# Kernel optimization log

Hardware: AMD Instinct MI355X
Metric: run time of the kernel (lower is better)

Reference implementation:

```python
import jax, jax.numpy as jnp
import numpy as np

H = 128            # hidden_size; also the chunk length from torch.split(x, hidden_size)
NUM_CHUNKS = 4096  # B
INPUT_SIZE = 1
NUM_CLASSES = 1


def setup_inputs() -> dict:
    key = jax.random.key(0)
    ks = jax.random.split(key, 7)
    N = NUM_CHUNKS * H
    s = 1.0 / np.sqrt(H).astype(np.float32)
    x = jax.random.normal(ks[0], (N,), dtype=jnp.float32)
    W_ih = jax.random.uniform(ks[1], (4 * H, INPUT_SIZE), minval=-s, maxval=s, dtype=jnp.float32)
    W_hh = jax.random.uniform(ks[2], (4 * H, H), minval=-s, maxval=s, dtype=jnp.float32)
    b_ih = jax.random.uniform(ks[3], (4 * H,), minval=-s, maxval=s, dtype=jnp.float32)
    b_hh = jax.random.uniform(ks[4], (4 * H,), minval=-s, maxval=s, dtype=jnp.float32)
    fc_W = jax.random.uniform(ks[5], (NUM_CLASSES, H), minval=-s, maxval=s, dtype=jnp.float32)
    fc_b = jax.random.uniform(ks[6], (NUM_CLASSES,), minval=-s, maxval=s, dtype=jnp.float32)
    return {"x": x, "W_ih": W_ih, "W_hh": W_hh, "b_ih": b_ih, "b_hh": b_hh,
            "fc_W": fc_W, "fc_b": fc_b}


def reference(x, W_ih, W_hh, b_ih, b_hh, fc_W, fc_b):
    # Original: split flat x into chunks of length H, run each chunk as a
    # batch-1 LSTM (input_size=1), take final hidden state, apply fc_out.
    # Here all chunks are batched into one fused recurrent pass.
    Hh = W_hh.shape[1]
    xb = x.reshape(-1, Hh, 1)                                  # [B, T=H, 1]
    # input projection is time-parallel: precompute gate pre-activations
    pre = jnp.einsum('bti,gi->btg', xb, W_ih) + b_ih + b_hh    # [B, T, 4H]

    def step(carry, p_t):
        h, c = carry                                           # [B, H] each
        gates = p_t + h @ W_hh.T                               # [B, 4H]
        i, f, g, o = jnp.split(gates, 4, axis=-1)              # PyTorch gate order i,f,g,o
        i = jax.nn.sigmoid(i)
        f = jax.nn.sigmoid(f)
        g = jnp.tanh(g)
        o = jax.nn.sigmoid(o)
        c = f * c + i * g
        h = o * jnp.tanh(c)
        return (h, c), None

    B = xb.shape[0]
    h0 = jnp.zeros((B, Hh), dtype=x.dtype)
    c0 = jnp.zeros((B, Hh), dtype=x.dtype)
    (hT, _), _ = jax.lax.scan(step, (h0, c0), jnp.swapaxes(pre, 0, 1))
    return hT @ fc_W.T + fc_b                                  # [B, num_classes]
```

## Files before the change

kernel.cpp:

```cpp
#include <hip/hip_runtime.h>


#define H   128
#define T   128
#define MB  16
#define BLOCK 512
#define HSTRIDE 136
#define XSTRIDE 20

typedef _Float16 f16x8 __attribute__((ext_vector_type(8)));
typedef float    f32x4 __attribute__((ext_vector_type(4)));

__global__ void prep_whh_kernel(const float* __restrict__ W_hh, _Float16* __restrict__ wfrag)
{
    int idx = blockIdx.x * blockDim.x + threadIdx.x;
    int l15 =  idx        & 15;
    int q   = (idx >> 4)  & 3;
    int kc  = (idx >> 6)  & 3;
    int g   = (idx >> 8)  & 3;
    int ct  = (idx >> 10) & 7;
    int n  = g * H + ct * 16 + l15;
    int k0 = kc * 32 + q * 8;
    const float* src = W_hh + (size_t)n * H + k0;
    f16x8 f;
    #pragma unroll
    for (int i = 0; i < 8; ++i) f[i] = (_Float16)src[i];
    *(f16x8*)(wfrag + (size_t)idx * 8) = f;
}

__device__ __forceinline__ float frcp(float v) { return __builtin_amdgcn_rcpf(v); }

__launch_bounds__(BLOCK, 2)
__global__ void lstm_fused_kernel(const float* __restrict__ x,
                                  const float* __restrict__ W_ih,
                                  const _Float16* __restrict__ wfrag,
                                  const float* __restrict__ b_ih,
                                  const float* __restrict__ b_hh,
                                  const float* __restrict__ fc_W,
                                  const float* __restrict__ fc_b,
                                  float* __restrict__ out)
{
    __shared__ __align__(16) float xs[T + 1][XSTRIDE];
    __shared__ __align__(16) _Float16 hbuf[2][MB][HSTRIDE];

    const int tid  = threadIdx.x;
    const int wave = tid >> 6;
    const int lane = tid & 63;
    const int l15  = lane & 15;
    const int q    = lane >> 4;
    const int jcol = wave * 16 + l15;

    {
        const int t0 = tid & 127;
        const int b0 = (tid >> 7) * 4;
        const float* xb = x + (size_t)blockIdx.x * (MB * T);
        #pragma unroll
        for (int bb = 0; bb < 4; ++bb)
            xs[t0][b0 + bb] = xb[(b0 + bb) * T + t0];
    }
    for (int i = tid; i < MB * HSTRIDE; i += BLOCK)
        (&hbuf[0][0][0])[i] = (_Float16)0.0f;

    f16x8 wf[4][4];
    {
        const _Float16* wbase = wfrag + (size_t)wave * (4 * 4 * 4 * 16 * 8);
        #pragma unroll
        for (int g = 0; g < 4; ++g)
            #pragma unroll
            for (int kc = 0; kc < 4; ++kc)
                wf[g][kc] = *(const f16x8*)(wbase + ((((g * 4 + kc) * 4 + q) * 16 + l15) * 8));
    }

    float wih[4], bias[4];
    #pragma unroll
    for (int g = 0; g < 4; ++g) {
        const int n = g * H + jcol;
        wih[g]  = W_ih[n];
        bias[g] = b_ih[n] + b_hh[n];
    }

    float c0[4] = {0.f, 0.f, 0.f, 0.f};

    __syncthreads();

    f32x4 initv[4];
    {
        float4 xl = *(const float4*)&xs[0][q * 4];
        #pragma unroll
        for (int g = 0; g < 4; ++g) {
            initv[g][0] = fmaf(xl.x, wih[g], bias[g]);
            initv[g][1] = fmaf(xl.y, wih[g], bias[g]);
            initv[g][2] = fmaf(xl.z, wih[g], bias[g]);
            initv[g][3] = fmaf(xl.w, wih[g], bias[g]);
        }
    }

    for (int t = 0; t < T; ++t) {
        #pragma unroll
        for (int g = 0; g < 4; ++g)
            #pragma unroll
            for (int kc = 0; kc < 4; ++kc)
                asm volatile("" : "+v"(wf[g][kc]));

        const int rb = t & 1;
        const int wb = rb ^ 1;

        f16x8 af[4];
        #pragma unroll
        for (int kc = 0; kc < 4; ++kc)
            af[kc] = *(const f16x8*)&hbuf[rb][l15][kc * 32 + q * 8];

        f32x4 acc[4];
        #pragma unroll
        for (int g = 0; g < 4; ++g)
            acc[g] = __builtin_amdgcn_mfma_f32_16x16x32_f16(af[0], wf[g][0], initv[g], 0, 0, 0);
        #pragma unroll
        for (int kc = 1; kc < 4; ++kc)
            #pragma unroll
            for (int g = 0; g < 4; ++g)
                acc[g] = __builtin_amdgcn_mfma_f32_16x16x32_f16(af[kc], wf[g][kc], acc[g], 0, 0, 0);

        {
            float4 xl = *(const float4*)&xs[t + 1][q * 4];
            #pragma unroll
            for (int g = 0; g < 4; ++g) {
                initv[g][0] = fmaf(xl.x, wih[g], bias[g]);
                initv[g][1] = fmaf(xl.y, wih[g], bias[g]);
                initv[g][2] = fmaf(xl.z, wih[g], bias[g]);
                initv[g][3] = fmaf(xl.w, wih[g], bias[g]);
            }
        }

        #pragma unroll
        for (int r = 0; r < 4; ++r) {
            const int b = q * 4 + r;
            float ai = acc[0][r], afv = acc[1][r], ag = acc[2][r], ao = acc[3][r];
            float Ei = __expf(-ai);
            float Ef = __expf(-afv);
            float Eg = __expf(2.0f * ag);
            float u  = 1.0f + Ei;
            float v  = 1.0f + Ef;
            float w  = 1.0f + Eg;
            float wm = Eg - 1.0f;
            float uw = u * w;
            float cn = fmaf(c0[r], uw, wm * v) * frcp(v * uw);
            c0[r] = cn;
            float Eo = __expf(-ao);
            float Ec = __expf(2.0f * cn);
            float hv = (Ec - 1.0f) * frcp((Ec + 1.0f) * (1.0f + Eo));
            hbuf[wb][b][jcol] = (_Float16)hv;
        }
        __syncthreads();
    }

    if (tid < 256) {
        const int b    = tid >> 4;
        const int part = tid & 15;
        const _Float16* hrow = &hbuf[0][b][0];
        float s = 0.0f;
        #pragma unroll
        for (int i = 0; i < 8; ++i) {
            const int j = part * 8 + i;
            s += fc_W[j] * (float)hrow[j];
        }
        s += __shfl_xor(s, 8, 16);
        s += __shfl_xor(s, 4, 16);
        s += __shfl_xor(s, 2, 16);
        s += __shfl_xor(s, 1, 16);
        if (part == 0)
            out[blockIdx.x * MB + b] = s + fc_b[0];
    }
}

extern "C" void kernel_launch(void* const* d_in, const int* in_sizes, int n_in,
                              void* d_out, int out_size, void* d_ws, size_t ws_size,
                              hipStream_t stream)
{
    const float* x    = (const float*)d_in[0];
    const float* W_ih = (const float*)d_in[1];
    const float* W_hh = (const float*)d_in[2];
    const float* b_ih = (const float*)d_in[3];
    const float* b_hh = (const float*)d_in[4];
    const float* fc_W = (const float*)d_in[5];
    const float* fc_b = (const float*)d_in[6];
    float* out = (float*)d_out;

    _Float16* wfrag = (_Float16*)d_ws;

    hipLaunchKernelGGL(prep_whh_kernel, dim3(32), dim3(256), 0, stream, W_hh, wfrag);

    const int B = in_sizes[0] / H;
    dim3 grid(B / MB);
    dim3 block(BLOCK);
    hipLaunchKernelGGL(lstm_fused_kernel, grid, block, 0, stream,
                       x, W_ih, wfrag, b_ih, b_hh, fc_W, fc_b, out);
}
```

Baseline: 173.8 us.

## Halve batch rows per block and dedupe per-lane gate math

Each block now handles 8 batch rows instead of 16, which doubles the grid so more blocks are resident per CU to hide the serial recurrence latency. The 16-row MFMA tile reads duplicated h rows, so half of the matrix math is wasted. The gate nonlinearities are deduplicated so each lane updates 2 cells instead of 4, shortening the per-step elementwise chain. Launch bounds are raised to 4 blocks per CU and the register-pinning asm on the weight fragments is removed, which risks spilling the 64 registers of resident weight fragments under the tighter register budget.

```diff
diff --git a/kernel.cpp b/kernel.cpp
--- a/kernel.cpp
+++ b/kernel.cpp
@@ -3,10 +3,10 @@
 
 #define H   128
 #define T   128
-#define MB  16
+#define MB  8
 #define BLOCK 512
 #define HSTRIDE 136
-#define XSTRIDE 20
+#define XSTRIDE 12
 
 typedef _Float16 f16x8 __attribute__((ext_vector_type(8)));
 typedef float    f32x4 __attribute__((ext_vector_type(4)));
@@ -30,7 +30,7 @@
 
 __device__ __forceinline__ float frcp(float v) { return __builtin_amdgcn_rcpf(v); }
 
-__launch_bounds__(BLOCK, 2)
+__launch_bounds__(BLOCK, 4)
 __global__ void lstm_fused_kernel(const float* __restrict__ x,
                                   const float* __restrict__ W_ih,
                                   const _Float16* __restrict__ wfrag,
@@ -50,13 +50,15 @@
     const int q    = lane >> 4;
     const int jcol = wave * 16 + l15;
 
+    const int r0 = (q >> 1) * 2;
+    const int b0 = (q * 4 + r0) & 7;
+
     {
         const int t0 = tid & 127;
-        const int b0 = (tid >> 7) * 4;
+        const int bb = tid >> 7;
         const float* xb = x + (size_t)blockIdx.x * (MB * T);
-        #pragma unroll
-        for (int bb = 0; bb < 4; ++bb)
-            xs[t0][b0 + bb] = xb[(b0 + bb) * T + t0];
+        xs[t0][bb]     = xb[bb * T + t0];
+        xs[t0][bb + 4] = xb[(bb + 4) * T + t0];
     }
     for (int i = tid; i < MB * HSTRIDE; i += BLOCK)
         (&hbuf[0][0][0])[i] = (_Float16)0.0f;
@@ -79,36 +81,27 @@
         bias[g] = b_ih[n] + b_hh[n];
     }
 
-    float c0[4] = {0.f, 0.f, 0.f, 0.f};
+    float c0 = 0.f, c1 = 0.f;
 
     __syncthreads();
 
     f32x4 initv[4];
     {
-        float4 xl = *(const float4*)&xs[0][q * 4];
-        #pragma unroll
-        for (int g = 0; g < 4; ++g) {
-            initv[g][0] = fmaf(xl.x, wih[g], bias[g]);
-            initv[g][1] = fmaf(xl.y, wih[g], bias[g]);
-            initv[g][2] = fmaf(xl.z, wih[g], bias[g]);
-            initv[g][3] = fmaf(xl.w, wih[g], bias[g]);
-        }
+        #pragma unroll
+        for (int g = 0; g < 4; ++g)
+            #pragma unroll
+            for (int r = 0; r < 4; ++r)
+                initv[g][r] = fmaf(xs[0][(q * 4 + r) & 7], wih[g], bias[g]);
     }
 
     for (int t = 0; t < T; ++t) {
-        #pragma unroll
-        for (int g = 0; g < 4; ++g)
-            #pragma unroll
-            for (int kc = 0; kc < 4; ++kc)
-                asm volatile("" : "+v"(wf[g][kc]));
-
         const int rb = t & 1;
         const int wb = rb ^ 1;
 
         f16x8 af[4];
         #pragma unroll
         for (int kc = 0; kc < 4; ++kc)
-            af[kc] = *(const f16x8*)&hbuf[rb][l15][kc * 32 + q * 8];
+            af[kc] = *(const f16x8*)&hbuf[rb][l15 & 7][kc * 32 + q * 8];
 
         f32x4 acc[4];
         #pragma unroll
@@ -120,20 +113,14 @@
             for (int g = 0; g < 4; ++g)
                 acc[g] = __builtin_amdgcn_mfma_f32_16x16x32_f16(af[kc], wf[g][kc], acc[g], 0, 0, 0);
 
+        #pragma unroll
+        for (int g = 0; g < 4; ++g)
+            #pragma unroll
+            for (int r = 0; r < 4; ++r)
+                initv[g][r] = fmaf(xs[t + 1][(q * 4 + r) & 7], wih[g], bias[g]);
+
         {
-            float4 xl = *(const float4*)&xs[t + 1][q * 4];
-            #pragma unroll
-            for (int g = 0; g < 4; ++g) {
-                initv[g][0] = fmaf(xl.x, wih[g], bias[g]);
-                initv[g][1] = fmaf(xl.y, wih[g], bias[g]);
-                initv[g][2] = fmaf(xl.z, wih[g], bias[g]);
-                initv[g][3] = fmaf(xl.w, wih[g], bias[g]);
-            }
-        }
-
-        #pragma unroll
-        for (int r = 0; r < 4; ++r) {
-            const int b = q * 4 + r;
+            const int r = r0;
             float ai = acc[0][r], afv = acc[1][r], ag = acc[2][r], ao = acc[3][r];
             float Ei = __expf(-ai);
             float Ef = __expf(-afv);
@@ -143,17 +130,35 @@
             float w  = 1.0f + Eg;
             float wm = Eg - 1.0f;
             float uw = u * w;
-            float cn = fmaf(c0[r], uw, wm * v) * frcp(v * uw);
-            c0[r] = cn;
+            float cn = fmaf(c0, uw, wm * v) * frcp(v * uw);
+            c0 = cn;
             float Eo = __expf(-ao);
             float Ec = __expf(2.0f * cn);
             float hv = (Ec - 1.0f) * frcp((Ec + 1.0f) * (1.0f + Eo));
-            hbuf[wb][b][jcol] = (_Float16)hv;
+            hbuf[wb][b0][jcol] = (_Float16)hv;
+        }
+        {
+            const int r = r0 + 1;
+            float ai = acc[0][r], afv = acc[1][r], ag = acc[2][r], ao = acc[3][r];
+            float Ei = __expf(-ai);
+            float Ef = __expf(-afv);
+            float Eg = __expf(2.0f * ag);
+            float u  = 1.0f + Ei;
+            float v  = 1.0f + Ef;
+            float w  = 1.0f + Eg;
+            float wm = Eg - 1.0f;
+            float uw = u * w;
+            float cn = fmaf(c1, uw, wm * v) * frcp(v * uw);
+            c1 = cn;
+            float Eo = __expf(-ao);
+            float Ec = __expf(2.0f * cn);
+            float hv = (Ec - 1.0f) * frcp((Ec + 1.0f) * (1.0f + Eo));
+            hbuf[wb][b0 + 1][jcol] = (_Float16)hv;
         }
         __syncthreads();
     }
 
-    if (tid < 256) {
+    if (tid < 128) {
         const int b    = tid >> 4;
         const int part = tid & 15;
         const _Float16* hrow = &hbuf[0][b][0];
```

Result: slower. 217.1 us (+24.9%).

## Split block into two ping-pong teams overlapping MFMA and gate math

Applied to the files above, without the earlier changes.

The 16 sequences in a block are split into two teams of 8, each served by 4 waves that own 2 column tiles. In each half-step one team runs the recurrent MFMAs while the other runs the elementwise gate nonlinearities, so matrix and vector work overlap across teams. The cost is twice the W_hh fragments in registers per wave, half-utilized MFMA rows (only 8 of 16 batch rows are real), and two barriers per timestep instead of one.

```diff
diff --git a/kernel.cpp b/kernel.cpp
--- a/kernel.cpp
+++ b/kernel.cpp
@@ -3,10 +3,9 @@
 
 #define H   128
 #define T   128
-#define MB  16
 #define BLOCK 512
 #define HSTRIDE 136
-#define XSTRIDE 20
+#define XSTRIDE 18
 
 typedef _Float16 f16x8 __attribute__((ext_vector_type(8)));
 typedef float    f32x4 __attribute__((ext_vector_type(4)));
@@ -30,6 +29,67 @@
 
 __device__ __forceinline__ float frcp(float v) { return __builtin_amdgcn_rcpf(v); }
 
+#define MFMA_STEP(tt)                                                             \
+    do {                                                                          \
+        const _Float16* hb = &hbuf[team][(tt) & 1][0][0];                         \
+        f16x8 af[4];                                                              \
+        _Pragma("unroll")                                                         \
+        for (int kc = 0; kc < 4; ++kc)                                            \
+            af[kc] = *(const f16x8*)(hb + (l15 & 7) * HSTRIDE + kc * 32 + q * 8); \
+        _Pragma("unroll")                                                         \
+        for (int ctl = 0; ctl < 2; ++ctl) {                                       \
+            _Pragma("unroll")                                                     \
+            for (int g = 0; g < 4; ++g) {                                         \
+                f32x4 iv;                                                         \
+                _Pragma("unroll")                                                 \
+                for (int r = 0; r < 4; ++r)                                       \
+                    iv[r] = fmaf(xs[tt][xrow + ((q * 4 + r) & 7)],                \
+                                 wih[ctl][g], bias[ctl][g]);                      \
+                acc[ctl][g] = __builtin_amdgcn_mfma_f32_16x16x32_f16(             \
+                    af[0], wf[ctl][g][0], iv, 0, 0, 0);                           \
+            }                                                                     \
+        }                                                                         \
+        _Pragma("unroll")                                                         \
+        for (int kc = 1; kc < 4; ++kc)                                            \
+            _Pragma("unroll")                                                     \
+            for (int ctl = 0; ctl < 2; ++ctl)                                     \
+                _Pragma("unroll")                                                 \
+                for (int g = 0; g < 4; ++g)                                       \
+                    acc[ctl][g] = __builtin_amdgcn_mfma_f32_16x16x32_f16(         \
+                        af[kc], wf[ctl][g][kc], acc[ctl][g], 0, 0, 0);            \
+    } while (0)
+
+#define EW_STEP(tt)                                                               \
+    do {                                                                          \
+        _Float16* hw = &hbuf[team][((tt) + 1) & 1][0][0];                         \
+        _Pragma("unroll")                                                         \
+        for (int ctl = 0; ctl < 2; ++ctl) {                                       \
+            const int jc = (ct0 + ctl) * 16 + l15;                                \
+            _Pragma("unroll")                                                     \
+            for (int rr = 0; rr < 2; ++rr) {                                      \
+                const int r = r0 + rr;                                            \
+                float ai  = acc[ctl][0][r];                                       \
+                float afv = acc[ctl][1][r];                                       \
+                float ag  = acc[ctl][2][r];                                       \
+                float ao  = acc[ctl][3][r];                                       \
+                float Ei = __expf(-ai);                                           \
+                float Ef = __expf(-afv);                                          \
+                float Eg = __expf(2.0f * ag);                                     \
+                float u  = 1.0f + Ei;                                             \
+                float v  = 1.0f + Ef;                                             \
+                float w  = 1.0f + Eg;                                             \
+                float wm = Eg - 1.0f;                                             \
+                float uw = u * w;                                                 \
+                float cn = fmaf(cst[ctl][rr], uw, wm * v) * frcp(v * uw);         \
+                cst[ctl][rr] = cn;                                                \
+                float Eo = __expf(-ao);                                           \
+                float Ec = __expf(2.0f * cn);                                     \
+                float hv = (Ec - 1.0f) * frcp((Ec + 1.0f) * (1.0f + Eo));         \
+                hw[(b0 + rr) * HSTRIDE + jc] = (_Float16)hv;                      \
+            }                                                                     \
+        }                                                                         \
+    } while (0)
+
 __launch_bounds__(BLOCK, 2)
 __global__ void lstm_fused_kernel(const float* __restrict__ x,
                                   const float* __restrict__ W_ih,
@@ -41,122 +101,79 @@
                                   float* __restrict__ out)
 {
     __shared__ __align__(16) float xs[T + 1][XSTRIDE];
-    __shared__ __align__(16) _Float16 hbuf[2][MB][HSTRIDE];
+    __shared__ __align__(16) _Float16 hbuf[2][2][8][HSTRIDE];
 
     const int tid  = threadIdx.x;
     const int wave = tid >> 6;
     const int lane = tid & 63;
     const int l15  = lane & 15;
     const int q    = lane >> 4;
-    const int jcol = wave * 16 + l15;
+    const int team = wave >> 2;
+    const int wt   = wave & 3;
+    const int ct0  = wt * 2;
+    const int xrow = team * 8;
+
+    const int r0 = (q >> 1) * 2;
+    const int b0 = (q * 4 + r0) & 7;
 
     {
         const int t0 = tid & 127;
-        const int b0 = (tid >> 7) * 4;
-        const float* xb = x + (size_t)blockIdx.x * (MB * T);
+        const int bb = tid >> 7;
+        const float* xb = x + (size_t)blockIdx.x * (16 * T);
+        xs[t0][bb]      = xb[bb * T + t0];
+        xs[t0][bb + 4]  = xb[(bb + 4) * T + t0];
+        xs[t0][bb + 8]  = xb[(bb + 8) * T + t0];
+        xs[t0][bb + 12] = xb[(bb + 12) * T + t0];
+    }
+    for (int i = tid; i < 8 * HSTRIDE; i += BLOCK) {
+        (&hbuf[0][0][0][0])[i] = (_Float16)0.0f;
+        (&hbuf[1][0][0][0])[i] = (_Float16)0.0f;
+    }
+
+    f16x8 wf[2][4][4];
+    float wih[2][4], bias[2][4];
+    #pragma unroll
+    for (int ctl = 0; ctl < 2; ++ctl) {
+        const _Float16* wbase = wfrag + (size_t)(ct0 + ctl) * 8192;
         #pragma unroll
-        for (int bb = 0; bb < 4; ++bb)
-            xs[t0][b0 + bb] = xb[(b0 + bb) * T + t0];
-    }
-    for (int i = tid; i < MB * HSTRIDE; i += BLOCK)
-        (&hbuf[0][0][0])[i] = (_Float16)0.0f;
-
-    f16x8 wf[4][4];
-    {
-        const _Float16* wbase = wfrag + (size_t)wave * (4 * 4 * 4 * 16 * 8);
-        #pragma unroll
-        for (int g = 0; g < 4; ++g)
+        for (int g = 0; g < 4; ++g) {
+            const int n = g * H + (ct0 + ctl) * 16 + l15;
+            wih[ctl][g]  = W_ih[n];
+            bias[ctl][g] = b_ih[n] + b_hh[n];
             #pragma unroll
             for (int kc = 0; kc < 4; ++kc)
-                wf[g][kc] = *(const f16x8*)(wbase + ((((g * 4 + kc) * 4 + q) * 16 + l15) * 8));
-    }
-
-    float wih[4], bias[4];
-    #pragma unroll
-    for (int g = 0; g < 4; ++g) {
-        const int n = g * H + jcol;
-        wih[g]  = W_ih[n];
-        bias[g] = b_ih[n] + b_hh[n];
-    }
-
-    float c0[4] = {0.f, 0.f, 0.f, 0.f};
+                wf[ctl][g][kc] = *(const f16x8*)(wbase + ((((g * 4 + kc) * 4 + q) * 16 + l15) * 8));
+        }
+    }
+
+    float cst[2][2] = {{0.f, 0.f}, {0.f, 0.f}};
+    f32x4 acc[2][4];
 
     __syncthreads();
 
-    f32x4 initv[4];
-    {
-        float4 xl = *(const float4*)&xs[0][q * 4];
-        #pragma unroll
-        for (int g = 0; g < 4; ++g) {
-            initv[g][0] = fmaf(xl.x, wih[g], bias[g]);
-            initv[g][1] = fmaf(xl.y, wih[g], bias[g]);
-            initv[g][2] = fmaf(xl.z, wih[g], bias[g]);
-            initv[g][3] = fmaf(xl.w, wih[g], bias[g]);
-        }
-    }
-
     for (int t = 0; t < T; ++t) {
-        #pragma unroll
-        for (int g = 0; g < 4; ++g)
-            #pragma unroll
-            for (int kc = 0; kc < 4; ++kc)
-                asm volatile("" : "+v"(wf[g][kc]));
-
-        const int rb = t & 1;
-        const int wb = rb ^ 1;
-
-        f16x8 af[4];
-        #pragma unroll
-        for (int kc = 0; kc < 4; ++kc)
-            af[kc] = *(const f16x8*)&hbuf[rb][l15][kc * 32 + q * 8];
-
-        f32x4 acc[4];
-        #pragma unroll
-        for (int g = 0; g < 4; ++g)
-            acc[g] = __builtin_amdgcn_mfma_f32_16x16x32_f16(af[0], wf[g][0], initv[g], 0, 0, 0);
-        #pragma unroll
-        for (int kc = 1; kc < 4; ++kc)
-            #pragma unroll
-            for (int g = 0; g < 4; ++g)
-                acc[g] = __builtin_amdgcn_mfma_f32_16x16x32_f16(af[kc], wf[g][kc], acc[g], 0, 0, 0);
-
-        {
-            float4 xl = *(const float4*)&xs[t + 1][q * 4];
-            #pragma unroll
-            for (int g = 0; g < 4; ++g) {
-                initv[g][0] = fmaf(xl.x, wih[g], bias[g]);
-                initv[g][1] = fmaf(xl.y, wih[g], bias[g]);
-                initv[g][2] = fmaf(xl.z, wih[g], bias[g]);
-                initv[g][3] = fmaf(xl.w, wih[g], bias[g]);
-            }
-        }
-
-        #pragma unroll
-        for (int r = 0; r < 4; ++r) {
-            const int b = q * 4 + r;
-            float ai = acc[0][r], afv = acc[1][r], ag = acc[2][r], ao = acc[3][r];
-            float Ei = __expf(-ai);
-            float Ef = __expf(-afv);
-            float Eg = __expf(2.0f * ag);
-            float u  = 1.0f + Ei;
-            float v  = 1.0f + Ef;
-            float w  = 1.0f + Eg;
-            float wm = Eg - 1.0f;
-            float uw = u * w;
-            float cn = fmaf(c0[r], uw, wm * v) * frcp(v * uw);
-            c0[r] = cn;
-            float Eo = __expf(-ao);
-            float Ec = __expf(2.0f * cn);
-            float hv = (Ec - 1.0f) * frcp((Ec + 1.0f) * (1.0f + Eo));
-            hbuf[wb][b][jcol] = (_Float16)hv;
+        if (team == 0) {
+            MFMA_STEP(t);
+        } else if (t > 0) {
+            EW_STEP(t - 1);
         }
         __syncthreads();
-    }
+        if (team == 0) {
+            EW_STEP(t);
+        } else {
+            MFMA_STEP(t);
+        }
+        __syncthreads();
+    }
+    if (team == 1) {
+        EW_STEP(T - 1);
+    }
+    __syncthreads();
 
     if (tid < 256) {
         const int b    = tid >> 4;
         const int part = tid & 15;
-        const _Float16* hrow = &hbuf[0][b][0];
+        const _Float16* hrow = &hbuf[b >> 3][0][b & 7][0];
         float s = 0.0f;
         #pragma unroll
         for (int i = 0; i < 8; ++i) {
@@ -168,7 +185,7 @@
         s += __shfl_xor(s, 2, 16);
         s += __shfl_xor(s, 1, 16);
         if (part == 0)
-            out[blockIdx.x * MB + b] = s + fc_b[0];
+            out[blockIdx.x * 16 + b] = s + fc_b[0];
     }
 }
 
@@ -190,7 +207,7 @@
     hipLaunchKernelGGL(prep_whh_kernel, dim3(32), dim3(256), 0, stream, W_hh, wfrag);
 
     const int B = in_sizes[0] / H;
-    dim3 grid(B / MB);
+    dim3 grid(B / 16);
     dim3 block(BLOCK);
     hipLaunchKernelGGL(lstm_fused_kernel, grid, block, 0, stream,
                        x, W_ih, wfrag, b_ih, b_hh, fc_W, fc_b, out);
```

New measurement: 248.6 us. 1.43x slower.
